# Performance work log

Hardware: AMD Instinct MI355X
Metric: run time of the kernel (lower is better)

Reference implementation:

```python
import jax, jax.numpy as jnp
import numpy as np

B, T, D, V, E = 128, 256, 1024, 32000, 300


def setup_inputs() -> dict:
    key = jax.random.key(0)
    ks = jax.random.split(key, 9)
    s = lambda d: 1.0 / np.sqrt(d)
    return {
        "input_to_decoder": jax.random.randint(ks[0], (B, 1), 0, V),
        "encoder_output": jax.random.normal(ks[1], (B, T, D), jnp.float32) * s(D),
        "state_h": jax.random.normal(ks[2], (B, D), jnp.float32) * s(D),
        "state_c": jax.random.normal(ks[3], (B, D), jnp.float32) * s(D),
        "emb_table": jax.random.normal(ks[4], (V, E), jnp.float32) * 0.02,
        "W_lstm": jax.random.normal(ks[5], (D + E, 4 * D), jnp.float32) * s(D + E),
        "U_lstm": jax.random.normal(ks[6], (D, 4 * D), jnp.float32) * s(D),
        "b_lstm": jnp.zeros((4 * D,), jnp.float32),
        "W_dense": jax.random.normal(ks[7], (D, V), jnp.float32) * s(D),
        "b_dense": jnp.zeros((V,), jnp.float32),
    }


def reference(input_to_decoder, encoder_output, state_h, state_c,
              emb_table, W_lstm, U_lstm, b_lstm, W_dense, b_dense):
    # embedding lookup + squeeze(axis=1): [B,1] -> [B,E]
    emb = emb_table[input_to_decoder[:, 0]]
    # Bahdanau-style dot scores: [B,T]
    scores = jnp.einsum("btd,bd->bt", encoder_output, state_h)
    # NOTE: faithful to source - context uses RAW (pre-softmax) scores
    context = jnp.einsum("btd,bt->bd", encoder_output, scores)  # [B,D]
    attention_weights = jax.nn.softmax(scores, axis=1)[..., None]  # [B,T,1]
    # concat context + embedding, single LSTM cell step (Keras gate order i,f,g,o)
    x = jnp.concatenate([context, emb], axis=1)  # [B,D+E]
    z = x @ W_lstm + state_h @ U_lstm + b_lstm  # [B,4D]
    zi, zf, zg, zo = jnp.split(z, 4, axis=1)
    c_new = jax.nn.sigmoid(zf) * state_c + jax.nn.sigmoid(zi) * jnp.tanh(zg)
    h_new = jax.nn.sigmoid(zo) * jnp.tanh(c_new)
    logits = h_new @ W_dense + b_dense  # [B,V]
    return logits, h_new, c_new, attention_weights, context
```

## Files before the change

### kernel.cpp

```cpp
#include <hip/hip_runtime.h>
#include <hip/hip_bf16.h>
#include <cmath>


#define Bc 128
#define Tc 256
#define Dc 1024
#define Vc 32000
#define Ec 300
#define KREAL 2348
#define KXP 2688
#define KSPLIT 7
#define N4 4096

typedef __attribute__((ext_vector_type(8))) short bf16x8;
typedef __attribute__((ext_vector_type(4))) float f32x4;

static __device__ __forceinline__ short f2bf(float x) {
    __hip_bfloat16 b = __float2bfloat16(x);
    return *reinterpret_cast<short*>(&b);
}
static __device__ __forceinline__ unsigned pack2(float a, float b) {
    return (unsigned)(unsigned short)f2bf(a) | ((unsigned)(unsigned short)f2bf(b) << 16);
}

__global__ void k_att1(const float* __restrict__ enc, const float* __restrict__ h,
                       float* __restrict__ scores_g, float* __restrict__ ctx_part) {
    const int tc = blockIdx.x;
    const int b  = blockIdx.y;
    const int tid = threadIdx.x;
    const int wave = tid >> 6, lane = tid & 63;
    __shared__ float s_acc[4][1024];

    const float4* h4 = (const float4*)(h + ((size_t)b << 10));
    float4 hv0 = h4[lane], hv1 = h4[lane + 64], hv2 = h4[lane + 128], hv3 = h4[lane + 192];

    float4 a0 = {0,0,0,0}, a1 = {0,0,0,0}, a2 = {0,0,0,0}, a3 = {0,0,0,0};
    const int t0 = (tc << 6) + (wave << 4);
    const float4* e4 = (const float4*)(enc + ((size_t)(b * Tc + t0) << 10));

    #pragma unroll 2
    for (int i = 0; i < 16; ++i) {
        float4 e0 = e4[lane], e1 = e4[lane + 64], e2 = e4[lane + 128], e3 = e4[lane + 192];
        e4 += 256;
        float d = e0.x*hv0.x + e0.y*hv0.y + e0.z*hv0.z + e0.w*hv0.w
                + e1.x*hv1.x + e1.y*hv1.y + e1.z*hv1.z + e1.w*hv1.w
                + e2.x*hv2.x + e2.y*hv2.y + e2.z*hv2.z + e2.w*hv2.w
                + e3.x*hv3.x + e3.y*hv3.y + e3.z*hv3.z + e3.w*hv3.w;
        #pragma unroll
        for (int off = 32; off; off >>= 1) d += __shfl_xor(d, off, 64);
        if (lane == 0) scores_g[(b << 8) + t0 + i] = d;
        a0.x += d*e0.x; a0.y += d*e0.y; a0.z += d*e0.z; a0.w += d*e0.w;
        a1.x += d*e1.x; a1.y += d*e1.y; a1.z += d*e1.z; a1.w += d*e1.w;
        a2.x += d*e2.x; a2.y += d*e2.y; a2.z += d*e2.z; a2.w += d*e2.w;
        a3.x += d*e3.x; a3.y += d*e3.y; a3.z += d*e3.z; a3.w += d*e3.w;
    }

    *(float4*)&s_acc[wave][lane << 2]         = a0;
    *(float4*)&s_acc[wave][256 + (lane << 2)] = a1;
    *(float4*)&s_acc[wave][512 + (lane << 2)] = a2;
    *(float4*)&s_acc[wave][768 + (lane << 2)] = a3;
    __syncthreads();
    float4 r0 = *(const float4*)&s_acc[0][tid << 2];
    float4 r1 = *(const float4*)&s_acc[1][tid << 2];
    float4 r2 = *(const float4*)&s_acc[2][tid << 2];
    float4 r3 = *(const float4*)&s_acc[3][tid << 2];
    float4 r;
    r.x = r0.x + r1.x + r2.x + r3.x;
    r.y = r0.y + r1.y + r2.y + r3.y;
    r.z = r0.z + r1.z + r2.z + r3.z;
    r.w = r0.w + r1.w + r2.w + r3.w;
    *(float4*)(ctx_part + (((size_t)(tc << 7) + b) << 10) + (tid << 2)) = r;
}

__global__ void k_att2(const float* __restrict__ ctx_part, const float* __restrict__ scores_g,
                       const int* __restrict__ idx, const float* __restrict__ emb_table,
                       const float* __restrict__ h,
                       float* __restrict__ ctx_out, float* __restrict__ attn_out,
                       unsigned short* __restrict__ x_bf) {
    const int b = blockIdx.x;
    const int tid = threadIdx.x;
    __shared__ float red[256];

    float4 cv = {0.f, 0.f, 0.f, 0.f};
    #pragma unroll
    for (int tc = 0; tc < 4; ++tc) {
        float4 s = *(const float4*)(ctx_part + (((size_t)(tc << 7) + b) << 10) + (tid << 2));
        cv.x += s.x; cv.y += s.y; cv.z += s.z; cv.w += s.w;
    }
    *(float4*)(ctx_out + ((size_t)b << 10) + (tid << 2)) = cv;

    unsigned short* xb = x_bf + (size_t)b * KXP;
    uint2 p0; p0.x = pack2(cv.x, cv.y); p0.y = pack2(cv.z, cv.w);
    *(uint2*)&xb[tid << 2] = p0;

    int row = idx[b];
    for (int i = tid; i < Ec; i += 256)
        xb[Dc + i] = (unsigned short)f2bf(emb_table[(size_t)row * Ec + i]);

    float4 hv = *(const float4*)(h + ((size_t)b << 10) + (tid << 2));
    uint2 p1; p1.x = pack2(hv.x, hv.y); p1.y = pack2(hv.z, hv.w);
    *(uint2*)&xb[(Dc + Ec) + (tid << 2)] = p1;

    for (int i = tid; i < KXP - KREAL; i += 256) xb[KREAL + i] = 0;

    float v = scores_g[(b << 8) + tid];
    red[tid] = v;
    __syncthreads();
    for (int s = 128; s; s >>= 1) { if (tid < s) red[tid] = fmaxf(red[tid], red[tid + s]); __syncthreads(); }
    float m = red[0];
    __syncthreads();
    float e = __expf(v - m);
    red[tid] = e;
    __syncthreads();
    for (int s = 128; s; s >>= 1) { if (tid < s) red[tid] += red[tid + s]; __syncthreads(); }
    attn_out[(b << 8) + tid] = e / red[0];
}

__global__ __launch_bounds__(512) void k_zgemm_mfma(
        const unsigned short* __restrict__ xbf, const float* __restrict__ Wl,
        const float* __restrict__ Ul, float* __restrict__ z_part) {
    __shared__ __align__(16) short blds[2 * 8 * 64 * 8];
    const int tid  = threadIdx.x;
    const int wid  = tid >> 6;
    const int lane = tid & 63;
    const int g    = lane >> 4;
    const int r    = lane & 15;
    const int n0   = blockIdx.x << 6;
    const int ksp  = blockIdx.y;

    const int pr = tid >> 4;
    const int c  = tid & 15;
    const int kk = (pr << 1) & 31;
    const int gg = kk >> 3, jj = kk & 7;
    const int ks0 = pr >> 4;

    f32x4 acc[4] = {};
    const unsigned short* xrow = xbf + (size_t)((wid << 4) + r) * KXP;

    float4 wra[2], wrb[2];
    bf16x8 areg[2][2];

    auto loadWU = [&](int gk) -> float4 {
        if (gk < 1324) return *(const float4*)(Wl + (size_t)gk * N4 + n0 + (c << 2));
        if (gk < KREAL) return *(const float4*)(Ul + (size_t)(gk - 1324) * N4 + n0 + (c << 2));
        return float4{0.f, 0.f, 0.f, 0.f};
    };

    {
        const int kt = (ksp * 6) << 6;
        wra[0] = loadWU(kt + (pr << 1));
        wrb[0] = loadWU(kt + (pr << 1) + 1);
        areg[0][0] = *(const bf16x8*)&xrow[kt + (g << 3)];
        areg[0][1] = *(const bf16x8*)&xrow[kt + 32 + (g << 3)];
    }

    #pragma unroll
    for (int t = 0; t < 6; ++t) {
        const int cur = t & 1;
        const int coff = cur << 12;
        {
            const float av[4] = {wra[cur].x, wra[cur].y, wra[cur].z, wra[cur].w};
            const float bv[4] = {wrb[cur].x, wrb[cur].y, wrb[cur].z, wrb[cur].w};
            #pragma unroll
            for (int i = 0; i < 4; ++i) {
                int n = (c << 2) + i;
                int nt = n >> 4;
                int inner = (gg << 4) | (n & 15);
                int Xs = ((((ks0 << 2) + nt) << 6) | inner) ^ nt;
                *(unsigned*)&blds[coff + (Xs << 3) + jj] = pack2(av[i], bv[i]);
            }
        }
        if (t < 5) {
            const int kt = ((ksp * 6) + t + 1) << 6;
            wra[cur ^ 1] = loadWU(kt + (pr << 1));
            wrb[cur ^ 1] = loadWU(kt + (pr << 1) + 1);
            areg[cur ^ 1][0] = *(const bf16x8*)&xrow[kt + (g << 3)];
            areg[cur ^ 1][1] = *(const bf16x8*)&xrow[kt + 32 + (g << 3)];
        }
        __syncthreads();
        #pragma unroll
        for (int ks = 0; ks < 2; ++ks) {
            #pragma unroll
            for (int nt = 0; nt < 4; ++nt) {
                int Xs = ((((ks << 2) + nt) << 6) | lane) ^ nt;
                bf16x8 bfr = *(const bf16x8*)&blds[coff + (Xs << 3)];
                acc[nt] = __builtin_amdgcn_mfma_f32_16x16x32_bf16(areg[cur][ks], bfr, acc[nt], 0, 0, 0);
            }
        }
    }

    float* zp = z_part + ((size_t)ksp << 19);
    #pragma unroll
    for (int nt = 0; nt < 4; ++nt) {
        int col = n0 + (nt << 4) + r;
        #pragma unroll
        for (int j = 0; j < 4; ++j) {
            int rowm = (wid << 4) + (g << 2) + j;
            zp[((size_t)rowm << 12) + col] = acc[nt][j];
        }
    }
}

__global__ void k_gates(const float* __restrict__ z_part, const float* __restrict__ b_lstm,
                        const float* __restrict__ c_in, float* __restrict__ h_new,
                        float* __restrict__ c_new, unsigned short* __restrict__ h_bf) {
    int i = blockIdx.x * 256 + threadIdx.x;
    int b = i >> 10, d = i & 1023;
    size_t base = ((size_t)b << 12) + d;
    float zi = b_lstm[d], zf = b_lstm[d + 1024], zg = b_lstm[d + 2048], zo = b_lstm[d + 3072];
    #pragma unroll
    for (int ks = 0; ks < KSPLIT; ++ks) {
        const float* zp = z_part + ((size_t)ks << 19);
        zi += zp[base];
        zf += zp[base + 1024];
        zg += zp[base + 2048];
        zo += zp[base + 3072];
    }
    float si = 1.f / (1.f + __expf(-zi));
    float sf = 1.f / (1.f + __expf(-zf));
    float so = 1.f / (1.f + __expf(-zo));
    float cn = sf * c_in[i] + si * tanhf(zg);
    float hn = so * tanhf(cn);
    c_new[i] = cn;
    h_new[i] = hn;
    h_bf[i] = (unsigned short)f2bf(hn);
}

__global__ __launch_bounds__(512) void k_logits_mfma(
        const unsigned short* __restrict__ hbf, const float* __restrict__ Wd,
        const float* __restrict__ bd, float* __restrict__ out) {
    __shared__ __align__(16) short blds[2 * 16 * 64 * 8];
    const int tid  = threadIdx.x;
    const int wid  = tid >> 6;
    const int lane = tid & 63;
    const int g    = lane >> 4;
    const int r    = lane & 15;
    const int n0   = blockIdx.x << 6;

    const int pr = tid >> 4;
    const int c  = tid & 15;
    const int kk = (pr << 1) & 31;
    const int gg = kk >> 3, jj = kk & 7;
    const int ksA = pr >> 4;
    const int ksB = ksA + 2;

    f32x4 acc[4] = {};
    const unsigned short* hrow = hbf + ((size_t)((wid << 4) + r) << 10);
    const float* wbase = Wd + (size_t)(pr << 1) * Vc + n0 + (c << 2);

    float4 wra[2], wrb[2], wrc[2], wrd[2];
    bf16x8 areg[2][4];

    {
        wra[0] = *(const float4*)(wbase);
        wrb[0] = *(const float4*)(wbase + Vc);
        wrc[0] = *(const float4*)(wbase + (size_t)64 * Vc);
        wrd[0] = *(const float4*)(wbase + (size_t)65 * Vc);
        #pragma unroll
        for (int ks = 0; ks < 4; ++ks)
            areg[0][ks] = *(const bf16x8*)&hrow[(ks << 5) + (g << 3)];
    }

    #pragma unroll
    for (int t = 0; t < 8; ++t) {
        const int cur = t & 1;
        const int coff = cur << 13;
        {
            const float a0[4] = {wra[cur].x, wra[cur].y, wra[cur].z, wra[cur].w};
            const float b0[4] = {wrb[cur].x, wrb[cur].y, wrb[cur].z, wrb[cur].w};
            const float c0[4] = {wrc[cur].x, wrc[cur].y, wrc[cur].z, wrc[cur].w};
            const float d0[4] = {wrd[cur].x, wrd[cur].y, wrd[cur].z, wrd[cur].w};
            #pragma unroll
            for (int i = 0; i < 4; ++i) {
                int n = (c << 2) + i;
                int nt = n >> 4;
                int inner = (gg << 4) | (n & 15);
                int XsA = ((((ksA << 2) + nt) << 6) | inner) ^ nt;
                int XsB = ((((ksB << 2) + nt) << 6) | inner) ^ nt;
                *(unsigned*)&blds[coff + (XsA << 3) + jj] = pack2(a0[i], b0[i]);
                *(unsigned*)&blds[coff + (XsB << 3) + jj] = pack2(c0[i], d0[i]);
            }
        }
        if (t < 7) {
            const float* wb2 = wbase + (size_t)((t + 1) << 7) * Vc;
            wra[cur ^ 1] = *(const float4*)(wb2);
            wrb[cur ^ 1] = *(const float4*)(wb2 + Vc);
            wrc[cur ^ 1] = *(const float4*)(wb2 + (size_t)64 * Vc);
            wrd[cur ^ 1] = *(const float4*)(wb2 + (size_t)65 * Vc);
            #pragma unroll
            for (int ks = 0; ks < 4; ++ks)
                areg[cur ^ 1][ks] = *(const bf16x8*)&hrow[((t + 1) << 7) + (ks << 5) + (g << 3)];
        }
        __syncthreads();
        #pragma unroll
        for (int ks = 0; ks < 4; ++ks) {
            #pragma unroll
            for (int nt = 0; nt < 4; ++nt) {
                int Xs = ((((ks << 2) + nt) << 6) | lane) ^ nt;
                bf16x8 bfr = *(const bf16x8*)&blds[coff + (Xs << 3)];
                acc[nt] = __builtin_amdgcn_mfma_f32_16x16x32_bf16(areg[cur][ks], bfr, acc[nt], 0, 0, 0);
            }
        }
    }

    #pragma unroll
    for (int nt = 0; nt < 4; ++nt) {
        int col = n0 + (nt << 4) + r;
        float bias = bd[col];
        #pragma unroll
        for (int j = 0; j < 4; ++j) {
            int row = (wid << 4) + (g << 2) + j;
            out[(size_t)row * Vc + col] = acc[nt][j] + bias;
        }
    }
}

extern "C" void kernel_launch(void* const* d_in, const int* in_sizes, int n_in,
                              void* d_out, int out_size, void* d_ws, size_t ws_size,
                              hipStream_t stream) {
    const int*   idx = (const int*)d_in[0];
    const float* enc = (const float*)d_in[1];
    const float* h   = (const float*)d_in[2];
    const float* c   = (const float*)d_in[3];
    const float* emb = (const float*)d_in[4];
    const float* Wl  = (const float*)d_in[5];
    const float* Ul  = (const float*)d_in[6];
    const float* bl  = (const float*)d_in[7];
    const float* Wd  = (const float*)d_in[8];
    const float* bd  = (const float*)d_in[9];

    float* out    = (float*)d_out;
    float* logits = out;
    float* h_new  = out + 4096000;
    float* c_new  = out + 4227072;
    float* attn   = out + 4358144;
    float* ctx    = out + 4390912;

    float*          ctx_part = out;
    float*          scores_g = out + 524288;
    float*          z_part   = out;
    unsigned short* x_bf16   = (unsigned short*)d_ws;
    unsigned short* h_bf16   = (unsigned short*)d_ws + 344064;

    hipLaunchKernelGGL(k_att1, dim3(4, 128), dim3(256), 0, stream, enc, h, scores_g, ctx_part);
    hipLaunchKernelGGL(k_att2, dim3(128), dim3(256), 0, stream, ctx_part, scores_g, idx, emb, h,
                       ctx, attn, x_bf16);
    hipLaunchKernelGGL(k_zgemm_mfma, dim3(64, KSPLIT), dim3(512), 0, stream, x_bf16, Wl, Ul, z_part);
    hipLaunchKernelGGL(k_gates, dim3(512), dim3(256), 0, stream, z_part, bl, c, h_new, c_new, h_bf16);
    hipLaunchKernelGGL(k_logits_mfma, dim3(500), dim3(512), 0, stream, h_bf16, Wd, bd, logits);
}
```

Before: 91.15 us.

## Fuse attention kernels into one 1024-thread block per batch; vectorize gates

Merges the two attention kernels into a single kernel with one 1024-thread block per batch row. The kernel keeps scores and the context partials in shared memory instead of writing them to global scratch and reading them back, which also removes one launch. The gates kernel now handles four elements per thread with float4 loads and stores. The risk is lower parallelism: attention drops from 512 blocks to 128 large blocks, on a GPU with many CUs, and uses 64KB+ of LDS per block.

```diff
diff --git a/kernel.cpp b/kernel.cpp
--- a/kernel.cpp
+++ b/kernel.cpp
@@ -24,19 +24,23 @@
     return (unsigned)(unsigned short)f2bf(a) | ((unsigned)(unsigned short)f2bf(b) << 16);
 }
 
-__global__ void k_att1(const float* __restrict__ enc, const float* __restrict__ h,
-                       float* __restrict__ scores_g, float* __restrict__ ctx_part) {
-    const int tc = blockIdx.x;
-    const int b  = blockIdx.y;
+__global__ __launch_bounds__(1024) void k_att(
+        const float* __restrict__ enc, const float* __restrict__ h,
+        const int* __restrict__ idx, const float* __restrict__ emb_table,
+        float* __restrict__ ctx_out, float* __restrict__ attn_out,
+        unsigned short* __restrict__ x_bf) {
+    const int b = blockIdx.x;
     const int tid = threadIdx.x;
     const int wave = tid >> 6, lane = tid & 63;
-    __shared__ float s_acc[4][1024];
+    __shared__ float s_acc[16][1024];
+    __shared__ float s_sc[256];
+    __shared__ float red[256];
 
     const float4* h4 = (const float4*)(h + ((size_t)b << 10));
     float4 hv0 = h4[lane], hv1 = h4[lane + 64], hv2 = h4[lane + 128], hv3 = h4[lane + 192];
 
     float4 a0 = {0,0,0,0}, a1 = {0,0,0,0}, a2 = {0,0,0,0}, a3 = {0,0,0,0};
-    const int t0 = (tc << 6) + (wave << 4);
+    const int t0 = wave << 4;
     const float4* e4 = (const float4*)(enc + ((size_t)(b * Tc + t0) << 10));
 
     #pragma unroll 2
@@ -49,72 +53,55 @@
                 + e3.x*hv3.x + e3.y*hv3.y + e3.z*hv3.z + e3.w*hv3.w;
         #pragma unroll
         for (int off = 32; off; off >>= 1) d += __shfl_xor(d, off, 64);
-        if (lane == 0) scores_g[(b << 8) + t0 + i] = d;
+        if (lane == 0) s_sc[t0 + i] = d;
         a0.x += d*e0.x; a0.y += d*e0.y; a0.z += d*e0.z; a0.w += d*e0.w;
         a1.x += d*e1.x; a1.y += d*e1.y; a1.z += d*e1.z; a1.w += d*e1.w;
         a2.x += d*e2.x; a2.y += d*e2.y; a2.z += d*e2.z; a2.w += d*e2.w;
         a3.x += d*e3.x; a3.y += d*e3.y; a3.z += d*e3.z; a3.w += d*e3.w;
     }
-
     *(float4*)&s_acc[wave][lane << 2]         = a0;
     *(float4*)&s_acc[wave][256 + (lane << 2)] = a1;
     *(float4*)&s_acc[wave][512 + (lane << 2)] = a2;
     *(float4*)&s_acc[wave][768 + (lane << 2)] = a3;
     __syncthreads();
-    float4 r0 = *(const float4*)&s_acc[0][tid << 2];
-    float4 r1 = *(const float4*)&s_acc[1][tid << 2];
-    float4 r2 = *(const float4*)&s_acc[2][tid << 2];
-    float4 r3 = *(const float4*)&s_acc[3][tid << 2];
-    float4 r;
-    r.x = r0.x + r1.x + r2.x + r3.x;
-    r.y = r0.y + r1.y + r2.y + r3.y;
-    r.z = r0.z + r1.z + r2.z + r3.z;
-    r.w = r0.w + r1.w + r2.w + r3.w;
-    *(float4*)(ctx_part + (((size_t)(tc << 7) + b) << 10) + (tid << 2)) = r;
-}
-
-__global__ void k_att2(const float* __restrict__ ctx_part, const float* __restrict__ scores_g,
-                       const int* __restrict__ idx, const float* __restrict__ emb_table,
-                       const float* __restrict__ h,
-                       float* __restrict__ ctx_out, float* __restrict__ attn_out,
-                       unsigned short* __restrict__ x_bf) {
-    const int b = blockIdx.x;
-    const int tid = threadIdx.x;
-    __shared__ float red[256];
-
-    float4 cv = {0.f, 0.f, 0.f, 0.f};
-    #pragma unroll
-    for (int tc = 0; tc < 4; ++tc) {
-        float4 s = *(const float4*)(ctx_part + (((size_t)(tc << 7) + b) << 10) + (tid << 2));
-        cv.x += s.x; cv.y += s.y; cv.z += s.z; cv.w += s.w;
-    }
-    *(float4*)(ctx_out + ((size_t)b << 10) + (tid << 2)) = cv;
+
+    float cv = 0.f;
+    #pragma unroll
+    for (int w = 0; w < 16; ++w) cv += s_acc[w][tid];
+    ctx_out[((size_t)b << 10) + tid] = cv;
+    s_acc[0][tid] = cv;
+    __syncthreads();
 
     unsigned short* xb = x_bf + (size_t)b * KXP;
-    uint2 p0; p0.x = pack2(cv.x, cv.y); p0.y = pack2(cv.z, cv.w);
-    *(uint2*)&xb[tid << 2] = p0;
-
-    int row = idx[b];
-    for (int i = tid; i < Ec; i += 256)
+    if (tid < 512) {
+        *(unsigned*)&xb[tid << 1] = pack2(s_acc[0][tid << 1], s_acc[0][(tid << 1) + 1]);
+        float2 hp = *(const float2*)(h + ((size_t)b << 10) + (tid << 1));
+        *(unsigned*)&xb[(Dc + Ec) + (tid << 1)] = pack2(hp.x, hp.y);
+    } else if (tid < 812) {
+        int i = tid - 512;
+        int row = idx[b];
         xb[Dc + i] = (unsigned short)f2bf(emb_table[(size_t)row * Ec + i]);
-
-    float4 hv = *(const float4*)(h + ((size_t)b << 10) + (tid << 2));
-    uint2 p1; p1.x = pack2(hv.x, hv.y); p1.y = pack2(hv.z, hv.w);
-    *(uint2*)&xb[(Dc + Ec) + (tid << 2)] = p1;
-
-    for (int i = tid; i < KXP - KREAL; i += 256) xb[KREAL + i] = 0;
-
-    float v = scores_g[(b << 8) + tid];
-    red[tid] = v;
-    __syncthreads();
-    for (int s = 128; s; s >>= 1) { if (tid < s) red[tid] = fmaxf(red[tid], red[tid + s]); __syncthreads(); }
+    } else if (tid < 812 + (KXP - KREAL)) {
+        xb[KREAL + (tid - 812)] = 0;
+    }
+
+    float v = (tid < 256) ? s_sc[tid] : -1e30f;
+    if (tid < 256) red[tid] = v;
+    __syncthreads();
+    for (int s = 128; s; s >>= 1) {
+        if (tid < s) red[tid] = fmaxf(red[tid], red[tid + s]);
+        __syncthreads();
+    }
     float m = red[0];
     __syncthreads();
     float e = __expf(v - m);
-    red[tid] = e;
-    __syncthreads();
-    for (int s = 128; s; s >>= 1) { if (tid < s) red[tid] += red[tid + s]; __syncthreads(); }
-    attn_out[(b << 8) + tid] = e / red[0];
+    if (tid < 256) red[tid] = e;
+    __syncthreads();
+    for (int s = 128; s; s >>= 1) {
+        if (tid < s) red[tid] += red[tid + s];
+        __syncthreads();
+    }
+    if (tid < 256) attn_out[(b << 8) + tid] = e / red[0];
 }
 
 __global__ __launch_bounds__(512) void k_zgemm_mfma(
@@ -206,25 +193,37 @@
                         const float* __restrict__ c_in, float* __restrict__ h_new,
                         float* __restrict__ c_new, unsigned short* __restrict__ h_bf) {
     int i = blockIdx.x * 256 + threadIdx.x;
-    int b = i >> 10, d = i & 1023;
-    size_t base = ((size_t)b << 12) + d;
-    float zi = b_lstm[d], zf = b_lstm[d + 1024], zg = b_lstm[d + 2048], zo = b_lstm[d + 3072];
+    int b = i >> 8, d4 = (i & 255) << 2;
+    size_t base = ((size_t)b << 12) + d4;
+    float4 zi = *(const float4*)(b_lstm + d4);
+    float4 zf = *(const float4*)(b_lstm + d4 + 1024);
+    float4 zg = *(const float4*)(b_lstm + d4 + 2048);
+    float4 zo = *(const float4*)(b_lstm + d4 + 3072);
     #pragma unroll
     for (int ks = 0; ks < KSPLIT; ++ks) {
         const float* zp = z_part + ((size_t)ks << 19);
-        zi += zp[base];
-        zf += zp[base + 1024];
-        zg += zp[base + 2048];
-        zo += zp[base + 3072];
-    }
-    float si = 1.f / (1.f + __expf(-zi));
-    float sf = 1.f / (1.f + __expf(-zf));
-    float so = 1.f / (1.f + __expf(-zo));
-    float cn = sf * c_in[i] + si * tanhf(zg);
-    float hn = so * tanhf(cn);
-    c_new[i] = cn;
-    h_new[i] = hn;
-    h_bf[i] = (unsigned short)f2bf(hn);
+        float4 t;
+        t = *(const float4*)(zp + base);        zi.x += t.x; zi.y += t.y; zi.z += t.z; zi.w += t.w;
+        t = *(const float4*)(zp + base + 1024); zf.x += t.x; zf.y += t.y; zf.z += t.z; zf.w += t.w;
+        t = *(const float4*)(zp + base + 2048); zg.x += t.x; zg.y += t.y; zg.z += t.z; zg.w += t.w;
+        t = *(const float4*)(zp + base + 3072); zo.x += t.x; zo.y += t.y; zo.z += t.z; zo.w += t.w;
+    }
+    float4 cin = *(const float4*)(c_in + ((size_t)b << 10) + d4);
+    float4 cn, hn;
+    {
+        float si = 1.f/(1.f+__expf(-zi.x)), sf = 1.f/(1.f+__expf(-zf.x)), so = 1.f/(1.f+__expf(-zo.x));
+        cn.x = sf*cin.x + si*tanhf(zg.x); hn.x = so*tanhf(cn.x);
+        si = 1.f/(1.f+__expf(-zi.y)); sf = 1.f/(1.f+__expf(-zf.y)); so = 1.f/(1.f+__expf(-zo.y));
+        cn.y = sf*cin.y + si*tanhf(zg.y); hn.y = so*tanhf(cn.y);
+        si = 1.f/(1.f+__expf(-zi.z)); sf = 1.f/(1.f+__expf(-zf.z)); so = 1.f/(1.f+__expf(-zo.z));
+        cn.z = sf*cin.z + si*tanhf(zg.z); hn.z = so*tanhf(cn.z);
+        si = 1.f/(1.f+__expf(-zi.w)); sf = 1.f/(1.f+__expf(-zf.w)); so = 1.f/(1.f+__expf(-zo.w));
+        cn.w = sf*cin.w + si*tanhf(zg.w); hn.w = so*tanhf(cn.w);
+    }
+    *(float4*)(c_new + ((size_t)b << 10) + d4) = cn;
+    *(float4*)(h_new + ((size_t)b << 10) + d4) = hn;
+    uint2 hp; hp.x = pack2(hn.x, hn.y); hp.y = pack2(hn.z, hn.w);
+    *(uint2*)&h_bf[((size_t)b << 10) + d4] = hp;
 }
 
 __global__ __launch_bounds__(512) void k_logits_mfma(
@@ -337,16 +336,12 @@
     float* attn   = out + 4358144;
     float* ctx    = out + 4390912;
 
-    float*          ctx_part = out;
-    float*          scores_g = out + 524288;
-    float*          z_part   = out;
-    unsigned short* x_bf16   = (unsigned short*)d_ws;
-    unsigned short* h_bf16   = (unsigned short*)d_ws + 344064;
-
-    hipLaunchKernelGGL(k_att1, dim3(4, 128), dim3(256), 0, stream, enc, h, scores_g, ctx_part);
-    hipLaunchKernelGGL(k_att2, dim3(128), dim3(256), 0, stream, ctx_part, scores_g, idx, emb, h,
-                       ctx, attn, x_bf16);
+    float*          z_part = out;
+    unsigned short* x_bf16 = (unsigned short*)d_ws;
+    unsigned short* h_bf16 = (unsigned short*)d_ws + 344064;
+
+    hipLaunchKernelGGL(k_att, dim3(128), dim3(1024), 0, stream, enc, h, idx, emb, ctx, attn, x_bf16);
     hipLaunchKernelGGL(k_zgemm_mfma, dim3(64, KSPLIT), dim3(512), 0, stream, x_bf16, Wl, Ul, z_part);
-    hipLaunchKernelGGL(k_gates, dim3(512), dim3(256), 0, stream, z_part, bl, c, h_new, c_new, h_bf16);
+    hipLaunchKernelGGL(k_gates, dim3(128), dim3(256), 0, stream, z_part, bl, c, h_new, c_new, h_bf16);
     hipLaunchKernelGGL(k_logits_mfma, dim3(500), dim3(512), 0, stream, h_bf16, Wd, bd, logits);
 }
```

New measurement: 92.23 us. No clear change (+1.2%).

## Fuse attention reduction and LSTM gates into producers via last-block atomic counters

Applied to the files above, without the earlier changes.

The attention partial kernel and the softmax/context/pack kernel become one kernel. The last of the four time-chunk blocks per batch row, found with an atomic counter and thread fences, does the final reduction. The same pattern folds the LSTM gate kernel into the split-K z GEMM: the last of 28 blocks per 64-column slice sums the partials and applies the gates. This removes two kernel launches and their inter-kernel gaps, but adds a counter memset. It also moves the gate work onto only 16 tail blocks, which serialises a memory-heavy reduction with little parallelism.

```diff
diff --git a/kernel.cpp b/kernel.cpp
--- a/kernel.cpp
+++ b/kernel.cpp
@@ -24,13 +24,18 @@
     return (unsigned)(unsigned short)f2bf(a) | ((unsigned)(unsigned short)f2bf(b) << 16);
 }
 
-__global__ void k_att1(const float* __restrict__ enc, const float* __restrict__ h,
-                       float* __restrict__ scores_g, float* __restrict__ ctx_part) {
+__global__ void k_att1f(const float* __restrict__ enc, const float* __restrict__ h,
+                        const int* __restrict__ idx, const float* __restrict__ emb_table,
+                        float* __restrict__ scores_g, float* __restrict__ ctx_part,
+                        float* __restrict__ ctx_out, float* __restrict__ attn_out,
+                        unsigned short* __restrict__ x_bf, int* __restrict__ cnt) {
     const int tc = blockIdx.x;
     const int b  = blockIdx.y;
     const int tid = threadIdx.x;
     const int wave = tid >> 6, lane = tid & 63;
     __shared__ float s_acc[4][1024];
+    __shared__ float red[256];
+    __shared__ int s_last;
 
     const float4* h4 = (const float4*)(h + ((size_t)b << 10));
     float4 hv0 = h4[lane], hv1 = h4[lane + 64], hv2 = h4[lane + 128], hv3 = h4[lane + 192];
@@ -61,31 +66,29 @@
     *(float4*)&s_acc[wave][512 + (lane << 2)] = a2;
     *(float4*)&s_acc[wave][768 + (lane << 2)] = a3;
     __syncthreads();
-    float4 r0 = *(const float4*)&s_acc[0][tid << 2];
-    float4 r1 = *(const float4*)&s_acc[1][tid << 2];
-    float4 r2 = *(const float4*)&s_acc[2][tid << 2];
-    float4 r3 = *(const float4*)&s_acc[3][tid << 2];
-    float4 r;
-    r.x = r0.x + r1.x + r2.x + r3.x;
-    r.y = r0.y + r1.y + r2.y + r3.y;
-    r.z = r0.z + r1.z + r2.z + r3.z;
-    r.w = r0.w + r1.w + r2.w + r3.w;
-    *(float4*)(ctx_part + (((size_t)(tc << 7) + b) << 10) + (tid << 2)) = r;
-}
-
-__global__ void k_att2(const float* __restrict__ ctx_part, const float* __restrict__ scores_g,
-                       const int* __restrict__ idx, const float* __restrict__ emb_table,
-                       const float* __restrict__ h,
-                       float* __restrict__ ctx_out, float* __restrict__ attn_out,
-                       unsigned short* __restrict__ x_bf) {
-    const int b = blockIdx.x;
-    const int tid = threadIdx.x;
-    __shared__ float red[256];
+    {
+        float4 r0 = *(const float4*)&s_acc[0][tid << 2];
+        float4 r1 = *(const float4*)&s_acc[1][tid << 2];
+        float4 r2 = *(const float4*)&s_acc[2][tid << 2];
+        float4 r3 = *(const float4*)&s_acc[3][tid << 2];
+        float4 r;
+        r.x = r0.x + r1.x + r2.x + r3.x;
+        r.y = r0.y + r1.y + r2.y + r3.y;
+        r.z = r0.z + r1.z + r2.z + r3.z;
+        r.w = r0.w + r1.w + r2.w + r3.w;
+        *(float4*)(ctx_part + (((size_t)(tc << 7) + b) << 10) + (tid << 2)) = r;
+    }
+
+    __threadfence();
+    if (tid == 0) s_last = (atomicAdd(&cnt[b], 1) == 3);
+    __syncthreads();
+    if (!s_last) return;
+    __threadfence();
 
     float4 cv = {0.f, 0.f, 0.f, 0.f};
     #pragma unroll
-    for (int tc = 0; tc < 4; ++tc) {
-        float4 s = *(const float4*)(ctx_part + (((size_t)(tc << 7) + b) << 10) + (tid << 2));
+    for (int t4 = 0; t4 < 4; ++t4) {
+        float4 s = *(const float4*)(ctx_part + (((size_t)(t4 << 7) + b) << 10) + (tid << 2));
         cv.x += s.x; cv.y += s.y; cv.z += s.z; cv.w += s.w;
     }
     *(float4*)(ctx_out + ((size_t)b << 10) + (tid << 2)) = cv;
@@ -117,10 +120,14 @@
     attn_out[(b << 8) + tid] = e / red[0];
 }
 
-__global__ __launch_bounds__(512) void k_zgemm_mfma(
+__global__ __launch_bounds__(512) void k_zgf(
         const unsigned short* __restrict__ xbf, const float* __restrict__ Wl,
-        const float* __restrict__ Ul, float* __restrict__ z_part) {
+        const float* __restrict__ Ul, float* __restrict__ z_part,
+        const float* __restrict__ bl, const float* __restrict__ c_in,
+        float* __restrict__ h_new, float* __restrict__ c_new,
+        unsigned short* __restrict__ h_bf, int* __restrict__ cnt2) {
     __shared__ __align__(16) short blds[2 * 8 * 64 * 8];
+    __shared__ int s_last;
     const int tid  = threadIdx.x;
     const int wid  = tid >> 6;
     const int lane = tid & 63;
@@ -200,31 +207,39 @@
             zp[((size_t)rowm << 12) + col] = acc[nt][j];
         }
     }
-}
-
-__global__ void k_gates(const float* __restrict__ z_part, const float* __restrict__ b_lstm,
-                        const float* __restrict__ c_in, float* __restrict__ h_new,
-                        float* __restrict__ c_new, unsigned short* __restrict__ h_bf) {
-    int i = blockIdx.x * 256 + threadIdx.x;
-    int b = i >> 10, d = i & 1023;
-    size_t base = ((size_t)b << 12) + d;
-    float zi = b_lstm[d], zf = b_lstm[d + 1024], zg = b_lstm[d + 2048], zo = b_lstm[d + 3072];
-    #pragma unroll
-    for (int ks = 0; ks < KSPLIT; ++ks) {
-        const float* zp = z_part + ((size_t)ks << 19);
-        zi += zp[base];
-        zf += zp[base + 1024];
-        zg += zp[base + 2048];
-        zo += zp[base + 3072];
-    }
-    float si = 1.f / (1.f + __expf(-zi));
-    float sf = 1.f / (1.f + __expf(-zf));
-    float so = 1.f / (1.f + __expf(-zo));
-    float cn = sf * c_in[i] + si * tanhf(zg);
-    float hn = so * tanhf(cn);
-    c_new[i] = cn;
-    h_new[i] = hn;
-    h_bf[i] = (unsigned short)f2bf(hn);
+
+    const int db = blockIdx.x & 15;
+    __threadfence();
+    if (tid == 0) s_last = (atomicAdd(&cnt2[db], 1) == 27);
+    __syncthreads();
+    if (!s_last) return;
+    __threadfence();
+
+    const int dbase = db << 6;
+    #pragma unroll 2
+    for (int it = 0; it < 16; ++it) {
+        int i = (it << 9) + tid;
+        int b = i >> 6, dl = i & 63;
+        int d = dbase + dl;
+        size_t base = ((size_t)b << 12) + d;
+        float zi = bl[d], zf = bl[d + 1024], zg = bl[d + 2048], zo = bl[d + 3072];
+        #pragma unroll
+        for (int ks = 0; ks < KSPLIT; ++ks) {
+            const float* zq = z_part + ((size_t)ks << 19);
+            zi += zq[base];
+            zf += zq[base + 1024];
+            zg += zq[base + 2048];
+            zo += zq[base + 3072];
+        }
+        float si = 1.f / (1.f + __expf(-zi));
+        float sf = 1.f / (1.f + __expf(-zf));
+        float so = 1.f / (1.f + __expf(-zo));
+        float cn = sf * c_in[(b << 10) + d] + si * tanhf(zg);
+        float hn = so * tanhf(cn);
+        c_new[(b << 10) + d] = cn;
+        h_new[(b << 10) + d] = hn;
+        h_bf[(b << 10) + d] = (unsigned short)f2bf(hn);
+    }
 }
 
 __global__ __launch_bounds__(512) void k_logits_mfma(
@@ -342,11 +357,15 @@
     float*          z_part   = out;
     unsigned short* x_bf16   = (unsigned short*)d_ws;
     unsigned short* h_bf16   = (unsigned short*)d_ws + 344064;
-
-    hipLaunchKernelGGL(k_att1, dim3(4, 128), dim3(256), 0, stream, enc, h, scores_g, ctx_part);
-    hipLaunchKernelGGL(k_att2, dim3(128), dim3(256), 0, stream, ctx_part, scores_g, idx, emb, h,
-                       ctx, attn, x_bf16);
-    hipLaunchKernelGGL(k_zgemm_mfma, dim3(64, KSPLIT), dim3(512), 0, stream, x_bf16, Wl, Ul, z_part);
-    hipLaunchKernelGGL(k_gates, dim3(512), dim3(256), 0, stream, z_part, bl, c, h_new, c_new, h_bf16);
+    int*            cnt      = (int*)((char*)d_ws + 950272);
+    int*            cnt_att  = cnt;
+    int*            cnt_zg   = cnt + 128;
+
+    hipMemsetAsync(cnt, 0, 1024, stream);
+
+    hipLaunchKernelGGL(k_att1f, dim3(4, 128), dim3(256), 0, stream,
+                       enc, h, idx, emb, scores_g, ctx_part, ctx, attn, x_bf16, cnt_att);
+    hipLaunchKernelGGL(k_zgf, dim3(64, KSPLIT), dim3(512), 0, stream,
+                       x_bf16, Wl, Ul, z_part, bl, c, h_new, c_new, h_bf16, cnt_zg);
     hipLaunchKernelGGL(k_logits_mfma, dim3(500), dim3(512), 0, stream, h_bf16, Wd, bd, logits);
 }
```

New measurement: 313.1 us. +243.5%, slower.
